# Kernel tuning notes

Measured on AMD Instinct MI355X. Metric: run time of the kernel, lower is better.

Reference implementation:

```python
import jax, jax.numpy as jnp
import numpy as np

N = 131072      # number of RoIs (instances)
D = 1024        # in_channels
H = 1024        # hidden dim (hard-coded in module)
L = 4           # number of FPN levels / routed experts
STD = 0.01      # init std for all weights (biases zero)


def setup_inputs() -> dict:
    key = jax.random.key(0)
    k = jax.random.split(key, 5)
    x = jax.random.normal(k[0], (N, D), dtype=jnp.float32)
    levels = jax.random.randint(k[1], (N,), 0, L, dtype=jnp.int32)
    # Per-level MLP params, normal(std=0.01) weights, zero biases.
    W1 = jax.random.normal(k[2], (L, D, H), dtype=jnp.float32) * STD
    b1 = jnp.zeros((L, H), dtype=jnp.float32)
    W2 = jax.random.normal(k[3], (L, H, H), dtype=jnp.float32) * STD
    b2 = jnp.zeros((L, H), dtype=jnp.float32)
    W3 = jax.random.normal(k[4], (L, H, 1), dtype=jnp.float32) * STD
    b3 = jnp.zeros((L, 1), dtype=jnp.float32)
    return {"x": x, "levels": levels, "W1": W1, "b1": b1,
            "W2": W2, "b2": b2, "W3": W3, "b3": b3}


def reference(x, levels, W1, b1, W2, b2, W3, b3):
    # Hard-routed per-level 3-layer MLP (FC-ReLU x2 + FC), dropout in eval
    # mode (identity). Rows routed to level l get that level's MLP output;
    # implemented jit-compatibly with a fixed loop over the 4 levels and a
    # row mask instead of data-dependent gather/scatter.
    result = jnp.zeros((x.shape[0], 1), dtype=x.dtype)
    for lvl in range(L):
        h = jax.nn.relu(x @ W1[lvl] + b1[lvl])       # [N, H]
        h = jax.nn.relu(h @ W2[lvl] + b2[lvl])       # [N, H]
        out = h @ W3[lvl] + b3[lvl]                  # [N, 1]
        result = jnp.where((levels == lvl)[:, None], out, result)
    return result
```

## Files before the change

kernel.cpp:

```cpp
#include <hip/hip_runtime.h>

#define NROWS   131072
#define KDIM    1024
#define NLVL    4
#define SLOT_CAP 132096
#define NSB     516
#define NNB     4

#define OFF_IDX  1024ull
#define OFF_PART (OFF_IDX + (size_t)SLOT_CAP * 4)
#define OFF_WT1  (OFF_PART + (size_t)SLOT_CAP * 64)
#define OFF_WT2  (OFF_WT1 + 8388608ull)
#define OFF_XBF  (OFF_WT2 + 8388608ull)
#define OFF_H1   (OFF_XBF + 268435456ull)

typedef __bf16 bf16x8 __attribute__((ext_vector_type(8)));
typedef float f32x4 __attribute__((ext_vector_type(4)));
typedef unsigned short u16x4 __attribute__((ext_vector_type(4)));

__device__ __forceinline__ unsigned short f2bf(float f) {
  unsigned int u = __float_as_uint(f);
  u += 0x7fffu + ((u >> 16) & 1u);
  return (unsigned short)(u >> 16);
}

__device__ __forceinline__ void gld_lds16(const void* g, void* l) {
  __builtin_amdgcn_global_load_lds(
      (const __attribute__((address_space(1))) void*)g,
      (__attribute__((address_space(3))) void*)l, 16, 0, 0);
}


__global__ void k_hist(const int* __restrict__ levels, int n, int* __restrict__ meta) {
  __shared__ int h[NLVL];
  if (threadIdx.x < NLVL) h[threadIdx.x] = 0;
  __syncthreads();
  for (int t = blockIdx.x * blockDim.x + threadIdx.x; t < n; t += gridDim.x * blockDim.x)
    atomicAdd(&h[levels[t]], 1);
  __syncthreads();
  if (threadIdx.x < NLVL) atomicAdd(&meta[threadIdx.x], h[threadIdx.x]);
}

__global__ void k_seg(int* meta) {
  if (threadIdx.x == 0 && blockIdx.x == 0) {
    int s = 0;
    for (int l = 0; l < NLVL; ++l) {
      int pc = (meta[l] + 255) & ~255;
      meta[8 + l] = s;
      meta[12 + l] = pc;
      s += pc;
    }
  }
}

__global__ void k_scatter(const int* __restrict__ levels, int n,
                          int* __restrict__ meta, int* __restrict__ idx) {
  __shared__ int h[NLVL], base[NLVL], cur[NLVL];
  int t = blockIdx.x * blockDim.x + threadIdx.x;
  if (threadIdx.x < NLVL) { h[threadIdx.x] = 0; cur[threadIdx.x] = 0; }
  __syncthreads();
  int lvl = 0;
  if (t < n) { lvl = levels[t]; atomicAdd(&h[lvl], 1); }
  __syncthreads();
  if (threadIdx.x < NLVL)
    base[threadIdx.x] = atomicAdd(&meta[4 + threadIdx.x], h[threadIdx.x]);
  __syncthreads();
  if (t < n) {
    int p = atomicAdd(&cur[lvl], 1);
    idx[meta[8 + lvl] + base[lvl] + p] = t;
  }
}

__global__ void k_cvt_x(const f32x4* __restrict__ x, u16x4* __restrict__ xb, int n4) {
  for (int t = blockIdx.x * blockDim.x + threadIdx.x; t < n4; t += gridDim.x * blockDim.x) {
    f32x4 v = x[t];
    u16x4 o;
    o[0] = f2bf(v[0]); o[1] = f2bf(v[1]); o[2] = f2bf(v[2]); o[3] = f2bf(v[3]);
    xb[t] = o;
  }
}

__global__ void k_twt(const float* __restrict__ W, unsigned short* __restrict__ Wt) {
  __shared__ float tile[32][33];
  int lvl = blockIdx.z;
  int k0 = blockIdx.x * 32, n0 = blockIdx.y * 32;
  int tx = threadIdx.x, ty = threadIdx.y;
  const float* Wp = W + (size_t)lvl * 1048576;
  unsigned short* Wtp = Wt + (size_t)lvl * 1048576;
#pragma unroll
  for (int i = 0; i < 4; ++i)
    tile[ty + i * 8][tx] = Wp[(size_t)(k0 + ty + i * 8) * 1024 + n0 + tx];
  __syncthreads();
#pragma unroll
  for (int i = 0; i < 4; ++i) {
    int nn = ty + i * 8;
    Wtp[(size_t)(n0 + nn) * 1024 + k0 + tx] = f2bf(tile[tx][nn]);
  }
}

#define BARRM   asm volatile("s_barrier" ::: "memory")
#define WAIT_L4 asm volatile("s_waitcnt lgkmcnt(4)" ::: "memory")
#define WAIT_L0 asm volatile("s_waitcnt lgkmcnt(0)" ::: "memory")
#define WAIT_V2 asm volatile("s_waitcnt vmcnt(2)" ::: "memory")
#define WAIT_V0 asm volatile("s_waitcnt vmcnt(0)" ::: "memory")
#define SB0     __builtin_amdgcn_sched_barrier(0)
#define PRIO(x) __builtin_amdgcn_s_setprio(x)

#define RDG1(p) { const char* w_ = lds + (p)*32768 + offW; \
                  const char* x_ = lds + (p)*32768 + offX; \
  wf[0] = *(const bf16x8*)(w_);        wf[1] = *(const bf16x8*)(w_ + 1024);  \
  xf[0] = *(const bf16x8*)(x_);        xf[1] = *(const bf16x8*)(x_ + 1024); }
#define RDG2(p) { const char* w_ = lds + (p)*32768 + offW; \
                  const char* x_ = lds + (p)*32768 + offX; \
  wf[2] = *(const bf16x8*)(w_ + 2048); wf[3] = *(const bf16x8*)(w_ + 3072); \
  xf[2] = *(const bf16x8*)(x_ + 2048); xf[3] = *(const bf16x8*)(x_ + 3072); }
#define MMA(nf_,mf_) acc[nf_][mf_] = __builtin_amdgcn_mfma_f32_16x16x32_bf16(wf[nf_], xf[mf_], acc[nf_][mf_], 0, 0, 0)
#define MMA_G1 { MMA(0,0); MMA(0,1); MMA(1,0); MMA(1,1); }
#define MMA_G2 { MMA(0,2); MMA(0,3); MMA(1,2); MMA(1,3); \
                 MMA(2,0); MMA(2,1); MMA(2,2); MMA(2,3); \
                 MMA(3,0); MMA(3,1); MMA(3,2); MMA(3,3); }
#define STG(p,t) { char* b_ = (char*)lds + (p)*32768 + (w << 10); \
  gld_lds16(xs0 + (t)*64, b_); \
  gld_lds16(ws0 + (t)*64, b_ + 16384); }

#define PHASE_CORE(p) \
  RDG1(p); RDG2(p); \
  WAIT_L4; SB0; \
  PRIO(1); MMA_G1; \
  WAIT_L0; SB0; \
  MMA_G2; PRIO(0);

template <int PASS>
__global__ __launch_bounds__(1024, 4) void k_gemm(
    const unsigned short* __restrict__ Asrc,
    const unsigned short* __restrict__ Wt,
    const float* __restrict__ bias,
    const float* __restrict__ w3,
    const int* __restrict__ meta,
    const int* __restrict__ idx,
    unsigned short* __restrict__ hout,
    float* __restrict__ partial) {
  __shared__ __align__(16) char lds[98304];

  const int bid = blockIdx.x;
  const int swz = (bid & 7) * (NSB * NNB / 8) + (bid >> 3);
  const int nb = swz & 3;
  const int sb = swz >> 2;
  const int slotbase = sb * 256;
  if (slotbase >= meta[11] + meta[15]) return;
  int lvl;
  if      (slotbase < meta[9])  lvl = 0;
  else if (slotbase < meta[10]) lvl = 1;
  else if (slotbase < meta[11]) lvl = 2;
  else                          lvl = 3;

  const int tid = threadIdx.x;
  const int ln  = tid & 63;
  const int w   = tid >> 6;
  const int wm  = w & 3;
  const int wn  = w >> 2;
  const int l15 = ln & 15;

  const int srow = w * 16 + (ln >> 2);
  const int cch  = (ln & 3) ^ ((ln >> 3) & 3);
  int ar0;
  if (PASS == 1) ar0 = idx[slotbase + srow];
  else           ar0 = slotbase + srow;
  const char* xs0 = (const char*)Asrc + (size_t)ar0 * 2048 + cch * 16;
  const char* ws0 = (const char*)Wt + ((size_t)lvl << 21)
                    + (size_t)(nb * 256 + srow) * 2048 + cch * 16;

  const int xorc = ((ln >> 4) ^ ((l15 >> 1) & 3)) * 16;
  const int offX = (wm * 64 + l15) * 64 + xorc;
  const int offW = 16384 + (wn * 64 + l15) * 64 + xorc;

  const f32x4 vzero = {0.f, 0.f, 0.f, 0.f};
  f32x4 acc[4][4];
#pragma unroll
  for (int a = 0; a < 4; ++a)
#pragma unroll
    for (int b = 0; b < 4; ++b) acc[a][b] = vzero;
  bf16x8 wf[4], xf[4];

  STG(0, 0); STG(1, 1);
  WAIT_V2;
  BARRM;

#pragma unroll
  for (int t = 0; t < 30; ++t) {
    const int p  = t % 3;
    const int ps = (t + 2) % 3;
    STG(ps, t + 2);
    PHASE_CORE(p);
    WAIT_V2; BARRM;
  }

  PHASE_CORE(0);
  WAIT_V0; BARRM;
  PHASE_CORE(1);

  const float* bv = bias + lvl * 1024;
  const int n_lo = (ln >> 4) * 4;

  if (PASS == 1) {
#pragma unroll
    for (int nf = 0; nf < 4; ++nf) {
#pragma unroll
      for (int mf = 0; mf < 4; ++mf) {
        int slot = slotbase + wm * 64 + mf * 16 + l15;
        int col = nb * 256 + wn * 64 + nf * 16 + n_lo;
        f32x4 bb = *(const f32x4*)&bv[col];
        f32x4 v = acc[nf][mf];
        u16x4 o;
#pragma unroll
        for (int r = 0; r < 4; ++r) o[r] = f2bf(fmaxf(v[r] + bb[r], 0.f));
        *(u16x4*)&hout[(size_t)slot * 1024 + col] = o;
      }
    }
  } else {
    const float* w3v = w3 + lvl * 1024;
    float ps4[4] = {0.f, 0.f, 0.f, 0.f};
#pragma unroll
    for (int mf = 0; mf < 4; ++mf) {
#pragma unroll
      for (int nf = 0; nf < 4; ++nf) {
        int col = nb * 256 + wn * 64 + nf * 16 + n_lo;
        f32x4 bb = *(const f32x4*)&bv[col];
        f32x4 ww = *(const f32x4*)&w3v[col];
        f32x4 v = acc[nf][mf];
#pragma unroll
        for (int r = 0; r < 4; ++r) ps4[mf] += fmaxf(v[r] + bb[r], 0.f) * ww[r];
      }
    }
#pragma unroll
    for (int mf = 0; mf < 4; ++mf) {
      float p = ps4[mf];
      p += __shfl_xor(p, 16);
      p += __shfl_xor(p, 32);
      if (ln < 16) {
        int slot = slotbase + wm * 64 + mf * 16 + ln;
        partial[(size_t)slot * 16 + nb * 4 + wn] = p;
      }
    }
  }
}

__global__ void k_final(const int* __restrict__ meta, const int* __restrict__ idx,
                        const float* __restrict__ partial, const float* __restrict__ b3,
                        float* __restrict__ out) {
  int t = blockIdx.x * blockDim.x + threadIdx.x;
  int total = meta[11] + meta[15];
  if (t >= total) return;
  int lvl;
  if (t < meta[9]) lvl = 0;
  else if (t < meta[10]) lvl = 1;
  else if (t < meta[11]) lvl = 2;
  else lvl = 3;
  int local = t - meta[8 + lvl];
  if (local >= meta[lvl]) return;
  int row = idx[t];
  const float* pp = partial + (size_t)t * 16;
  float s = 0.f;
#pragma unroll
  for (int j = 0; j < 16; ++j) s += pp[j];
  out[row] = s + b3[lvl];
}

extern "C" void kernel_launch(void* const* d_in, const int* in_sizes, int n_in,
                              void* d_out, int out_size, void* d_ws, size_t ws_size,
                              hipStream_t stream) {
  const float* x      = (const float*)d_in[0];
  const int*   levels = (const int*)d_in[1];
  const float* W1     = (const float*)d_in[2];
  const float* b1     = (const float*)d_in[3];
  const float* W2     = (const float*)d_in[4];
  const float* b2     = (const float*)d_in[5];
  const float* W3     = (const float*)d_in[6];
  const float* b3     = (const float*)d_in[7];
  float* out = (float*)d_out;

  char* ws = (char*)d_ws;
  int* meta = (int*)ws;
  int* idx = (int*)(ws + OFF_IDX);
  float* partial = (float*)(ws + OFF_PART);
  unsigned short* Wt1 = (unsigned short*)(ws + OFF_WT1);
  unsigned short* Wt2 = (unsigned short*)(ws + OFF_WT2);
  unsigned short* xb  = (unsigned short*)(ws + OFF_XBF);
  unsigned short* h1  = (unsigned short*)(ws + OFF_H1);

  hipMemsetAsync(d_ws, 0, OFF_IDX + (size_t)SLOT_CAP * 4, stream);
  k_hist<<<256, 256, 0, stream>>>(levels, NROWS, meta);
  k_seg<<<1, 64, 0, stream>>>(meta);
  k_scatter<<<512, 256, 0, stream>>>(levels, NROWS, meta, idx);
  k_cvt_x<<<2048, 256, 0, stream>>>((const f32x4*)x, (u16x4*)xb, NROWS * (KDIM / 4));
  k_twt<<<dim3(32, 32, 4), dim3(32, 8), 0, stream>>>(W1, Wt1);
  k_twt<<<dim3(32, 32, 4), dim3(32, 8), 0, stream>>>(W2, Wt2);

  k_gemm<1><<<NSB * NNB, 1024, 0, stream>>>(xb, Wt1, b1, nullptr, meta, idx, h1, nullptr);
  k_gemm<2><<<NSB * NNB, 1024, 0, stream>>>(h1, Wt2, b2, W3, meta, idx, nullptr, partial);

  k_final<<<516, 256, 0, stream>>>(meta, idx, partial, b3, out);
}
```

Measured before the change: 781.3 us.

## Halve GEMM block threads and double per-wave M tile to 128 rows

The block shrinks from 16 to 8 waves, arranged as 2 waves along M by 4 along N, so each wave now computes a 128x64 output tile with 32 accumulator fragments instead of 16. Each thread issues four global-to-LDS loads per stage instead of two, and the LDS fragment reads are regrouped so the W fragments are loaded once and reused across 8 X fragments. The aim is more MFMA work per LDS read and fewer waves competing for barriers. The cost is higher register pressure, with launch bounds changed to 512 threads and a minimum of 2 blocks, which may lower occupancy and reduce latency hiding.

```diff
diff --git a/kernel.cpp b/kernel.cpp
--- a/kernel.cpp
+++ b/kernel.cpp
@@ -101,37 +101,40 @@
 #define BARRM   asm volatile("s_barrier" ::: "memory")
 #define WAIT_L4 asm volatile("s_waitcnt lgkmcnt(4)" ::: "memory")
 #define WAIT_L0 asm volatile("s_waitcnt lgkmcnt(0)" ::: "memory")
-#define WAIT_V2 asm volatile("s_waitcnt vmcnt(2)" ::: "memory")
+#define WAIT_V4 asm volatile("s_waitcnt vmcnt(4)" ::: "memory")
 #define WAIT_V0 asm volatile("s_waitcnt vmcnt(0)" ::: "memory")
 #define SB0     __builtin_amdgcn_sched_barrier(0)
 #define PRIO(x) __builtin_amdgcn_s_setprio(x)
 
-#define RDG1(p) { const char* w_ = lds + (p)*32768 + offW; \
-                  const char* x_ = lds + (p)*32768 + offX; \
+#define RDW(p) { const char* w_ = lds + (p)*32768 + 16384 + offW; \
   wf[0] = *(const bf16x8*)(w_);        wf[1] = *(const bf16x8*)(w_ + 1024);  \
-  xf[0] = *(const bf16x8*)(x_);        xf[1] = *(const bf16x8*)(x_ + 1024); }
-#define RDG2(p) { const char* w_ = lds + (p)*32768 + offW; \
-                  const char* x_ = lds + (p)*32768 + offX; \
-  wf[2] = *(const bf16x8*)(w_ + 2048); wf[3] = *(const bf16x8*)(w_ + 3072); \
+  wf[2] = *(const bf16x8*)(w_ + 2048); wf[3] = *(const bf16x8*)(w_ + 3072); }
+#define RDX03(p) { const char* x_ = lds + (p)*32768 + offX; \
+  xf[0] = *(const bf16x8*)(x_);        xf[1] = *(const bf16x8*)(x_ + 1024); \
   xf[2] = *(const bf16x8*)(x_ + 2048); xf[3] = *(const bf16x8*)(x_ + 3072); }
+#define RDX47(p) { const char* x_ = lds + (p)*32768 + offX + 4096; \
+  xf[4] = *(const bf16x8*)(x_);        xf[5] = *(const bf16x8*)(x_ + 1024); \
+  xf[6] = *(const bf16x8*)(x_ + 2048); xf[7] = *(const bf16x8*)(x_ + 3072); }
 #define MMA(nf_,mf_) acc[nf_][mf_] = __builtin_amdgcn_mfma_f32_16x16x32_bf16(wf[nf_], xf[mf_], acc[nf_][mf_], 0, 0, 0)
-#define MMA_G1 { MMA(0,0); MMA(0,1); MMA(1,0); MMA(1,1); }
-#define MMA_G2 { MMA(0,2); MMA(0,3); MMA(1,2); MMA(1,3); \
-                 MMA(2,0); MMA(2,1); MMA(2,2); MMA(2,3); \
-                 MMA(3,0); MMA(3,1); MMA(3,2); MMA(3,3); }
+#define MMA_MH0 { _Pragma("unroll") for (int nf_ = 0; nf_ < 4; ++nf_) { \
+  MMA(nf_,0); MMA(nf_,1); MMA(nf_,2); MMA(nf_,3); } }
+#define MMA_MH1 { _Pragma("unroll") for (int nf_ = 0; nf_ < 4; ++nf_) { \
+  MMA(nf_,4); MMA(nf_,5); MMA(nf_,6); MMA(nf_,7); } }
 #define STG(p,t) { char* b_ = (char*)lds + (p)*32768 + (w << 10); \
   gld_lds16(xs0 + (t)*64, b_); \
-  gld_lds16(ws0 + (t)*64, b_ + 16384); }
+  gld_lds16(xs1 + (t)*64, b_ + 8192); \
+  gld_lds16(ws0 + (t)*64, b_ + 16384); \
+  gld_lds16(ws1 + (t)*64, b_ + 16384 + 8192); }
 
 #define PHASE_CORE(p) \
-  RDG1(p); RDG2(p); \
+  RDW(p); RDX03(p); SB0; RDX47(p); \
   WAIT_L4; SB0; \
-  PRIO(1); MMA_G1; \
+  PRIO(1); MMA_MH0; \
   WAIT_L0; SB0; \
-  MMA_G2; PRIO(0);
+  MMA_MH1; PRIO(0);
 
 template <int PASS>
-__global__ __launch_bounds__(1024, 4) void k_gemm(
+__global__ __launch_bounds__(512, 2) void k_gemm(
     const unsigned short* __restrict__ Asrc,
     const unsigned short* __restrict__ Wt,
     const float* __restrict__ bias,
@@ -157,33 +160,35 @@
   const int tid = threadIdx.x;
   const int ln  = tid & 63;
   const int w   = tid >> 6;
-  const int wm  = w & 3;
-  const int wn  = w >> 2;
+  const int wm  = w >> 2;
+  const int wn  = w & 3;
   const int l15 = ln & 15;
 
   const int srow = w * 16 + (ln >> 2);
   const int cch  = (ln & 3) ^ ((ln >> 3) & 3);
-  int ar0;
-  if (PASS == 1) ar0 = idx[slotbase + srow];
-  else           ar0 = slotbase + srow;
+  int ar0, ar1;
+  if (PASS == 1) { ar0 = idx[slotbase + srow]; ar1 = idx[slotbase + srow + 128]; }
+  else           { ar0 = slotbase + srow;      ar1 = slotbase + srow + 128; }
   const char* xs0 = (const char*)Asrc + (size_t)ar0 * 2048 + cch * 16;
+  const char* xs1 = (const char*)Asrc + (size_t)ar1 * 2048 + cch * 16;
   const char* ws0 = (const char*)Wt + ((size_t)lvl << 21)
                     + (size_t)(nb * 256 + srow) * 2048 + cch * 16;
+  const char* ws1 = ws0 + 128 * 2048;
 
   const int xorc = ((ln >> 4) ^ ((l15 >> 1) & 3)) * 16;
-  const int offX = (wm * 64 + l15) * 64 + xorc;
-  const int offW = 16384 + (wn * 64 + l15) * 64 + xorc;
+  const int offX = (wm * 128 + l15) * 64 + xorc;
+  const int offW = (wn * 64 + l15) * 64 + xorc;
 
   const f32x4 vzero = {0.f, 0.f, 0.f, 0.f};
-  f32x4 acc[4][4];
+  f32x4 acc[4][8];
 #pragma unroll
   for (int a = 0; a < 4; ++a)
 #pragma unroll
-    for (int b = 0; b < 4; ++b) acc[a][b] = vzero;
-  bf16x8 wf[4], xf[4];
+    for (int b = 0; b < 8; ++b) acc[a][b] = vzero;
+  bf16x8 wf[4], xf[8];
 
   STG(0, 0); STG(1, 1);
-  WAIT_V2;
+  WAIT_V4;
   BARRM;
 
 #pragma unroll
@@ -192,7 +197,7 @@
     const int ps = (t + 2) % 3;
     STG(ps, t + 2);
     PHASE_CORE(p);
-    WAIT_V2; BARRM;
+    WAIT_V4; BARRM;
   }
 
   PHASE_CORE(0);
@@ -206,8 +211,8 @@
 #pragma unroll
     for (int nf = 0; nf < 4; ++nf) {
 #pragma unroll
-      for (int mf = 0; mf < 4; ++mf) {
-        int slot = slotbase + wm * 64 + mf * 16 + l15;
+      for (int mf = 0; mf < 8; ++mf) {
+        int slot = slotbase + wm * 128 + mf * 16 + l15;
         int col = nb * 256 + wn * 64 + nf * 16 + n_lo;
         f32x4 bb = *(const f32x4*)&bv[col];
         f32x4 v = acc[nf][mf];
@@ -219,9 +224,9 @@
     }
   } else {
     const float* w3v = w3 + lvl * 1024;
-    float ps4[4] = {0.f, 0.f, 0.f, 0.f};
-#pragma unroll
-    for (int mf = 0; mf < 4; ++mf) {
+    float ps8[8] = {0.f, 0.f, 0.f, 0.f, 0.f, 0.f, 0.f, 0.f};
+#pragma unroll
+    for (int mf = 0; mf < 8; ++mf) {
 #pragma unroll
       for (int nf = 0; nf < 4; ++nf) {
         int col = nb * 256 + wn * 64 + nf * 16 + n_lo;
@@ -229,16 +234,16 @@
         f32x4 ww = *(const f32x4*)&w3v[col];
         f32x4 v = acc[nf][mf];
 #pragma unroll
-        for (int r = 0; r < 4; ++r) ps4[mf] += fmaxf(v[r] + bb[r], 0.f) * ww[r];
+        for (int r = 0; r < 4; ++r) ps8[mf] += fmaxf(v[r] + bb[r], 0.f) * ww[r];
       }
     }
 #pragma unroll
-    for (int mf = 0; mf < 4; ++mf) {
-      float p = ps4[mf];
+    for (int mf = 0; mf < 8; ++mf) {
+      float p = ps8[mf];
       p += __shfl_xor(p, 16);
       p += __shfl_xor(p, 32);
       if (ln < 16) {
-        int slot = slotbase + wm * 64 + mf * 16 + ln;
+        int slot = slotbase + wm * 128 + mf * 16 + ln;
         partial[(size_t)slot * 16 + nb * 4 + wn] = p;
       }
     }
@@ -296,8 +301,8 @@
   k_twt<<<dim3(32, 32, 4), dim3(32, 8), 0, stream>>>(W1, Wt1);
   k_twt<<<dim3(32, 32, 4), dim3(32, 8), 0, stream>>>(W2, Wt2);
 
-  k_gemm<1><<<NSB * NNB, 1024, 0, stream>>>(xb, Wt1, b1, nullptr, meta, idx, h1, nullptr);
-  k_gemm<2><<<NSB * NNB, 1024, 0, stream>>>(h1, Wt2, b2, W3, meta, idx, nullptr, partial);
+  k_gemm<1><<<NSB * NNB, 512, 0, stream>>>(xb, Wt1, b1, nullptr, meta, idx, h1, nullptr);
+  k_gemm<2><<<NSB * NNB, 512, 0, stream>>>(h1, Wt2, b2, W3, meta, idx, nullptr, partial);
 
   k_final<<<516, 256, 0, stream>>>(meta, idx, partial, b3, out);
 }
```

Result: slower. 806.7 us (+3.3%).

## Shrink GEMM tiles to 128x128 with 4 waves and double-buffered LDS

Applied to the files above, without the earlier changes.

The routed GEMM kernels move from 256x256 tiles with 16 waves and 96KB triple-buffered LDS to 128x128 tiles with 4 waves and 32KB double-buffered LDS. Per-level padding drops from 256 to 128 rows, so fewer padded rows are computed, and the smaller blocks allow more blocks per CU. In exchange, arithmetic intensity per tile is halved, global traffic for A and W is higher, and the shallower pipeline waits on all loads (vmcnt 0) every step, which exposes more load latency.

```diff
diff --git a/kernel.cpp b/kernel.cpp
--- a/kernel.cpp
+++ b/kernel.cpp
@@ -3,9 +3,9 @@
 #define NROWS   131072
 #define KDIM    1024
 #define NLVL    4
-#define SLOT_CAP 132096
-#define NSB     516
-#define NNB     4
+#define SLOT_CAP 131584
+#define NSB     1028
+#define NNB     8
 
 #define OFF_IDX  1024ull
 #define OFF_PART (OFF_IDX + (size_t)SLOT_CAP * 4)
@@ -45,7 +45,7 @@
   if (threadIdx.x == 0 && blockIdx.x == 0) {
     int s = 0;
     for (int l = 0; l < NLVL; ++l) {
-      int pc = (meta[l] + 255) & ~255;
+      int pc = (meta[l] + 127) & ~127;
       meta[8 + l] = s;
       meta[12 + l] = pc;
       s += pc;
@@ -101,37 +101,38 @@
 #define BARRM   asm volatile("s_barrier" ::: "memory")
 #define WAIT_L4 asm volatile("s_waitcnt lgkmcnt(4)" ::: "memory")
 #define WAIT_L0 asm volatile("s_waitcnt lgkmcnt(0)" ::: "memory")
-#define WAIT_V2 asm volatile("s_waitcnt vmcnt(2)" ::: "memory")
 #define WAIT_V0 asm volatile("s_waitcnt vmcnt(0)" ::: "memory")
 #define SB0     __builtin_amdgcn_sched_barrier(0)
 #define PRIO(x) __builtin_amdgcn_s_setprio(x)
 
-#define RDG1(p) { const char* w_ = lds + (p)*32768 + offW; \
-                  const char* x_ = lds + (p)*32768 + offX; \
-  wf[0] = *(const bf16x8*)(w_);        wf[1] = *(const bf16x8*)(w_ + 1024);  \
-  xf[0] = *(const bf16x8*)(x_);        xf[1] = *(const bf16x8*)(x_ + 1024); }
-#define RDG2(p) { const char* w_ = lds + (p)*32768 + offW; \
-                  const char* x_ = lds + (p)*32768 + offX; \
-  wf[2] = *(const bf16x8*)(w_ + 2048); wf[3] = *(const bf16x8*)(w_ + 3072); \
-  xf[2] = *(const bf16x8*)(x_ + 2048); xf[3] = *(const bf16x8*)(x_ + 3072); }
+#define RDG1(p) { const char* w_ = lds + (p)*16384 + 8192 + offW; \
+                  const char* x_ = lds + (p)*16384 + offX; \
+  wf[0] = *(const bf16x8*)(w_);        xf[0] = *(const bf16x8*)(x_); \
+  wf[1] = *(const bf16x8*)(w_ + 1024); xf[1] = *(const bf16x8*)(x_ + 1024); }
+#define RDG2(p) { const char* w_ = lds + (p)*16384 + 8192 + offW; \
+                  const char* x_ = lds + (p)*16384 + offX; \
+  wf[2] = *(const bf16x8*)(w_ + 2048); xf[2] = *(const bf16x8*)(x_ + 2048); \
+  wf[3] = *(const bf16x8*)(w_ + 3072); xf[3] = *(const bf16x8*)(x_ + 3072); }
 #define MMA(nf_,mf_) acc[nf_][mf_] = __builtin_amdgcn_mfma_f32_16x16x32_bf16(wf[nf_], xf[mf_], acc[nf_][mf_], 0, 0, 0)
 #define MMA_G1 { MMA(0,0); MMA(0,1); MMA(1,0); MMA(1,1); }
 #define MMA_G2 { MMA(0,2); MMA(0,3); MMA(1,2); MMA(1,3); \
                  MMA(2,0); MMA(2,1); MMA(2,2); MMA(2,3); \
                  MMA(3,0); MMA(3,1); MMA(3,2); MMA(3,3); }
-#define STG(p,t) { char* b_ = (char*)lds + (p)*32768 + (w << 10); \
+#define STG(p,t) { char* b_ = (char*)lds + (p)*16384 + (w * 2048); \
   gld_lds16(xs0 + (t)*64, b_); \
-  gld_lds16(ws0 + (t)*64, b_ + 16384); }
+  gld_lds16(xs1 + (t)*64, b_ + 1024); \
+  gld_lds16(ws0 + (t)*64, b_ + 8192); \
+  gld_lds16(ws1 + (t)*64, b_ + 8192 + 1024); }
 
 #define PHASE_CORE(p) \
-  RDG1(p); RDG2(p); \
+  RDG1(p); SB0; RDG2(p); \
   WAIT_L4; SB0; \
   PRIO(1); MMA_G1; \
   WAIT_L0; SB0; \
   MMA_G2; PRIO(0);
 
 template <int PASS>
-__global__ __launch_bounds__(1024, 4) void k_gemm(
+__global__ __launch_bounds__(256, 4) void k_gemm(
     const unsigned short* __restrict__ Asrc,
     const unsigned short* __restrict__ Wt,
     const float* __restrict__ bias,
@@ -140,13 +141,13 @@
     const int* __restrict__ idx,
     unsigned short* __restrict__ hout,
     float* __restrict__ partial) {
-  __shared__ __align__(16) char lds[98304];
+  __shared__ __align__(16) char lds[32768];
 
   const int bid = blockIdx.x;
   const int swz = (bid & 7) * (NSB * NNB / 8) + (bid >> 3);
-  const int nb = swz & 3;
-  const int sb = swz >> 2;
-  const int slotbase = sb * 256;
+  const int nb = swz & 7;
+  const int sb = swz >> 3;
+  const int slotbase = sb * 128;
   if (slotbase >= meta[11] + meta[15]) return;
   int lvl;
   if      (slotbase < meta[9])  lvl = 0;
@@ -157,22 +158,24 @@
   const int tid = threadIdx.x;
   const int ln  = tid & 63;
   const int w   = tid >> 6;
-  const int wm  = w & 3;
-  const int wn  = w >> 2;
+  const int wm  = w >> 1;
+  const int wn  = w & 1;
   const int l15 = ln & 15;
 
-  const int srow = w * 16 + (ln >> 2);
+  const int srow = w * 32 + (ln >> 2);
   const int cch  = (ln & 3) ^ ((ln >> 3) & 3);
-  int ar0;
-  if (PASS == 1) ar0 = idx[slotbase + srow];
-  else           ar0 = slotbase + srow;
+  int ar0, ar1;
+  if (PASS == 1) { ar0 = idx[slotbase + srow]; ar1 = idx[slotbase + srow + 16]; }
+  else           { ar0 = slotbase + srow;      ar1 = slotbase + srow + 16; }
   const char* xs0 = (const char*)Asrc + (size_t)ar0 * 2048 + cch * 16;
+  const char* xs1 = (const char*)Asrc + (size_t)ar1 * 2048 + cch * 16;
   const char* ws0 = (const char*)Wt + ((size_t)lvl << 21)
-                    + (size_t)(nb * 256 + srow) * 2048 + cch * 16;
+                    + (size_t)(nb * 128 + srow) * 2048 + cch * 16;
+  const char* ws1 = ws0 + 16 * 2048;
 
   const int xorc = ((ln >> 4) ^ ((l15 >> 1) & 3)) * 16;
   const int offX = (wm * 64 + l15) * 64 + xorc;
-  const int offW = 16384 + (wn * 64 + l15) * 64 + xorc;
+  const int offW = (wn * 64 + l15) * 64 + xorc;
 
   const f32x4 vzero = {0.f, 0.f, 0.f, 0.f};
   f32x4 acc[4][4];
@@ -182,21 +185,16 @@
     for (int b = 0; b < 4; ++b) acc[a][b] = vzero;
   bf16x8 wf[4], xf[4];
 
-  STG(0, 0); STG(1, 1);
-  WAIT_V2;
-  BARRM;
-
-#pragma unroll
-  for (int t = 0; t < 30; ++t) {
-    const int p  = t % 3;
-    const int ps = (t + 2) % 3;
-    STG(ps, t + 2);
+  STG(0, 0);
+  WAIT_V0; BARRM;
+
+#pragma unroll
+  for (int t = 0; t < 31; ++t) {
+    const int p = t & 1;
+    STG(p ^ 1, t + 1);
     PHASE_CORE(p);
-    WAIT_V2; BARRM;
-  }
-
-  PHASE_CORE(0);
-  WAIT_V0; BARRM;
+    WAIT_V0; BARRM;
+  }
   PHASE_CORE(1);
 
   const float* bv = bias + lvl * 1024;
@@ -208,7 +206,7 @@
 #pragma unroll
       for (int mf = 0; mf < 4; ++mf) {
         int slot = slotbase + wm * 64 + mf * 16 + l15;
-        int col = nb * 256 + wn * 64 + nf * 16 + n_lo;
+        int col = nb * 128 + wn * 64 + nf * 16 + n_lo;
         f32x4 bb = *(const f32x4*)&bv[col];
         f32x4 v = acc[nf][mf];
         u16x4 o;
@@ -224,7 +222,7 @@
     for (int mf = 0; mf < 4; ++mf) {
 #pragma unroll
       for (int nf = 0; nf < 4; ++nf) {
-        int col = nb * 256 + wn * 64 + nf * 16 + n_lo;
+        int col = nb * 128 + wn * 64 + nf * 16 + n_lo;
         f32x4 bb = *(const f32x4*)&bv[col];
         f32x4 ww = *(const f32x4*)&w3v[col];
         f32x4 v = acc[nf][mf];
@@ -239,7 +237,7 @@
       p += __shfl_xor(p, 32);
       if (ln < 16) {
         int slot = slotbase + wm * 64 + mf * 16 + ln;
-        partial[(size_t)slot * 16 + nb * 4 + wn] = p;
+        partial[(size_t)slot * 16 + nb * 2 + wn] = p;
       }
     }
   }
@@ -296,8 +294,8 @@
   k_twt<<<dim3(32, 32, 4), dim3(32, 8), 0, stream>>>(W1, Wt1);
   k_twt<<<dim3(32, 32, 4), dim3(32, 8), 0, stream>>>(W2, Wt2);
 
-  k_gemm<1><<<NSB * NNB, 1024, 0, stream>>>(xb, Wt1, b1, nullptr, meta, idx, h1, nullptr);
-  k_gemm<2><<<NSB * NNB, 1024, 0, stream>>>(h1, Wt2, b2, W3, meta, idx, nullptr, partial);
-
-  k_final<<<516, 256, 0, stream>>>(meta, idx, partial, b3, out);
-}
+  k_gemm<1><<<NSB * NNB, 256, 0, stream>>>(xb, Wt1, b1, nullptr, meta, idx, h1, nullptr);
+  k_gemm<2><<<NSB * NNB, 256, 0, stream>>>(h1, Wt2, b2, W3, meta, idx, nullptr, partial);
+
+  k_final<<<514, 256, 0, stream>>>(meta, idx, partial, b3, out);
+}
```

Result: slower. 821.8 us (+5.2%).
